# Optimization experiments

Measured on AMD Instinct MI355X. Metric: run time of the kernel, lower is better.

## Reference

```python
import jax, jax.numpy as jnp
import numpy as np

N_USERS = 200000
N_ITEMS = 100000
NNZ = 4000000
LATENT_DIM = 64
N_LAYERS = 3


def setup_inputs() -> dict:
    key = jax.random.key(0)
    k1, k2, k3, k4, k5 = jax.random.split(key, 5)
    N = N_USERS + N_ITEMS
    # nn.init.normal_(std=0.1) for both embedding tables
    user_emb = 0.1 * jax.random.normal(k1, (N_USERS, LATENT_DIM), dtype=jnp.float32)
    item_emb = 0.1 * jax.random.normal(k2, (N_ITEMS, LATENT_DIM), dtype=jnp.float32)
    # COO representation of the normalized sparse adjacency graph (getSparseGraph())
    vals = jax.random.uniform(k3, (NNZ,), dtype=jnp.float32)
    rows = jax.random.randint(k4, (NNZ,), 0, N, dtype=jnp.int32)
    cols = jax.random.randint(k5, (NNZ,), 0, N, dtype=jnp.int32)
    return {"user_emb": user_emb, "item_emb": item_emb, "vals": vals,
            "rows": rows, "cols": cols}


def reference(user_emb, item_emb, vals, rows, cols):
    """LightGCN.computer(): L rounds of SpMM propagation + mean over layers."""
    n_users = user_emb.shape[0]
    N = n_users + item_emb.shape[0]
    all_emb = jnp.concatenate([user_emb, item_emb], axis=0)  # [N, d]
    emb = all_emb
    acc = all_emb  # running sum of layer outputs (== mean of stacked embs * (L+1))
    for _ in range(N_LAYERS):
        # sparse.mm(G, emb): gather rows of emb at cols, scale by edge values,
        # scatter-add into destination rows.
        emb = jax.ops.segment_sum(vals[:, None] * emb[cols], rows, num_segments=N)
        acc = acc + emb
    light_out = acc / (N_LAYERS + 1)  # mean over (L+1) stacked layer embeddings
    users = light_out[:n_users]
    items = light_out[n_users:]
    return users, items
```

## Files before the change

kernel.cpp:

```cpp
#include <hip/hip_runtime.h>

#define N_USERS 200000
#define N_ITEMS 100000
#define NTOT    300000
#define NNZ     4000000
#define DIM     64
#define TOT_F   (NTOT * DIM)
#define TOT_F4  (TOT_F / 4)
#define USER_F4 ((N_USERS * DIM) / 4)

#define NCB     1172
#define CAP     3712
#define GPAD    16
#define NPB     250

typedef unsigned short ushort_t;
typedef unsigned long long u64_t;

__device__ __forceinline__ ushort_t f2bf(float f) {
    unsigned u = __float_as_uint(f);
    unsigned r = (u + 0x7FFFu + ((u >> 16) & 1u)) >> 16;
    return (ushort_t)r;
}

__global__ __launch_bounds__(256) void k_cvt(const float* __restrict__ ue,
                                             const float* __restrict__ ie,
                                             ushort_t* __restrict__ b0) {
    int i = blockIdx.x * blockDim.x + threadIdx.x;
    if (i >= TOT_F / 8) return;
    const float4* src = (i < USER_F4 / 2)
        ? reinterpret_cast<const float4*>(ue) + 2 * i
        : reinterpret_cast<const float4*>(ie) + 2 * i - USER_F4;
    float4 a = src[0], b = src[1];
    ushort_t o[8] = { f2bf(a.x), f2bf(a.y), f2bf(a.z), f2bf(a.w),
                      f2bf(b.x), f2bf(b.y), f2bf(b.z), f2bf(b.w) };
    reinterpret_cast<uint4*>(b0)[i] = *reinterpret_cast<uint4*>(o);
}


__global__ __launch_bounds__(256) void k_pb2(const int* __restrict__ rows,
                                             const int* __restrict__ cols,
                                             const float* __restrict__ vals,
                                             int* __restrict__ gcur,
                                             u64_t* __restrict__ bseg) {
    __shared__ int bh[NCB];
    int b = blockIdx.x, t = threadIdx.x;
    for (int i = t; i < NCB; i += 256) bh[i] = 0;
    __syncthreads();
    const int i0 = b * 4000, i1 = i0 + 4000;
    const int4* r4 = reinterpret_cast<const int4*>(rows);
    const int4* c4 = reinterpret_cast<const int4*>(cols);
    const float4* v4 = reinterpret_cast<const float4*>(vals);
    for (int i = i0 + t; i < i1; i += 256) {
        int4 r = r4[i];
        atomicAdd(&bh[r.x >> 8], 1);
        atomicAdd(&bh[r.y >> 8], 1);
        atomicAdd(&bh[r.z >> 8], 1);
        atomicAdd(&bh[r.w >> 8], 1);
    }
    __syncthreads();
    for (int k = t; k < NCB; k += 256) {
        int c = bh[k];
        bh[k] = c ? atomicAdd(&gcur[k * GPAD], c) : 0;
    }
    __syncthreads();
    for (int i = i0 + t; i < i1; i += 256) {
        int4   r = r4[i];
        int4   c = c4[i];
        float4 v = v4[i];
#define PUT(RR, CC, VV)                                                    \
        {                                                                  \
            int k = (RR) >> 8;                                             \
            int p = atomicAdd(&bh[k], 1);                                  \
            unsigned hi = (((unsigned)(RR) & 255u) << 24) | (unsigned)(CC);\
            bseg[(size_t)k * CAP + p] =                                    \
                ((u64_t)hi << 32) | (unsigned)__float_as_int(VV);          \
        }
        PUT(r.x, c.x, v.x)
        PUT(r.y, c.y, v.y)
        PUT(r.z, c.z, v.z)
        PUT(r.w, c.w, v.w)
#undef PUT
    }
}

__global__ __launch_bounds__(256) void k_rowsort(const int* __restrict__ gcur,
                                                 const u64_t* __restrict__ bseg,
                                                 long long* __restrict__ ecv,
                                                 int2* __restrict__ rstart2) {
    __shared__ int rh[256];
    __shared__ int rb[256];
    int b = blockIdx.x, t = threadIdx.x;
    int tot = gcur[b * GPAD];
    size_t segbase = (size_t)b * CAP;
    rh[t] = 0;
    __syncthreads();
    for (int e = t; e < tot; e += 256) {
        unsigned hi = (unsigned)(bseg[segbase + e] >> 32);
        atomicAdd(&rh[hi >> 24], 1);
    }
    __syncthreads();
    if (t == 0) {
        int run = 0;
        for (int i = 0; i < 256; ++i) { int c = rh[i]; rb[i] = run; run += c; }
    }
    __syncthreads();
    int row = b * 256 + t;
    if (row < NTOT)
        rstart2[row] = make_int2((int)segbase + rb[t],
                                 (int)segbase + rb[t] + rh[t]);
    rh[t] = rb[t];
    __syncthreads();
    for (int e = t; e < tot; e += 256) {
        u64_t q = bseg[segbase + e];
        unsigned hi = (unsigned)(q >> 32);
        int p = atomicAdd(&rh[hi >> 24], 1);
        ecv[segbase + p] = ((long long)((hi & 0x00FFFFFFu) << 7) << 32) |
                           (unsigned)q;
    }
    __syncthreads();
    if (t < 16 && tot + t < CAP) ecv[segbase + tot + t] = 0;
}


template<int LAYER>
__global__ __launch_bounds__(256) void k_spmm(const int2* __restrict__ rstart2,
                                              const long long* __restrict__ ecv,
                                              const ushort_t* __restrict__ src,
                                              const float* __restrict__ ue,
                                              const float* __restrict__ ie,
                                              ushort_t* __restrict__ dstb,
                                              float* __restrict__ out) {
    int wid  = blockIdx.x * 4 + (threadIdx.x >> 6);
    int lane = threadIdx.x & 63;
    if (wid >= NTOT) return;
    int2 se = rstart2[wid];
    int start = se.x, end = se.y;

    const int half = lane >> 5;
    const int d02  = (lane & 31) * 4;

    float acc0 = 0.f, acc1 = 0.f;
    long long q = ecv[start + (lane & 15)];
    for (int base = start; base < end; base += 16) {
        int rem = end - base;
        long long qn = q;
        if (rem > 16) qn = ecv[base + 16 + (lane & 15)];
        int qlo = (int)(unsigned)(q & 0xffffffffu);
        int qhi = (int)(unsigned)((unsigned long long)q >> 32);
        int remh = rem - half;
#pragma unroll
        for (int j = 0; j < 8; ++j) {
            int slot = 2 * j + half;
            float v  = __int_as_float(__shfl(qlo, slot));
            unsigned off = (unsigned)__shfl(qhi, slot);
            v = (2 * j < remh) ? v : 0.f;
            unsigned u = *reinterpret_cast<const unsigned*>(
                             reinterpret_cast<const char*>(src) + (off + d02));
            acc0 += v * __uint_as_float(u << 16);
            acc1 += v * __uint_as_float(u & 0xffff0000u);
        }
        q = qn;
    }

    acc0 += __shfl_xor(acc0, 32);
    acc1 += __shfl_xor(acc1, 32);

    if (lane < 32) {
        size_t o = (size_t)wid * DIM + (size_t)lane * 2;
        unsigned pk = ((unsigned)f2bf(acc1) << 16) | (unsigned)f2bf(acc0);
        if (LAYER == 1) {
            const float* bsrc = (wid < N_USERS)
                ? ue + o : ie + (o - (size_t)N_USERS * DIM);
            float2 b2 = *reinterpret_cast<const float2*>(bsrc);
            __builtin_nontemporal_store(b2.x + acc0, out + o);
            __builtin_nontemporal_store(b2.y + acc1, out + o + 1);
            *reinterpret_cast<unsigned*>(dstb + o) = pk;
        } else if (LAYER == 2) {
            float2 prev = *reinterpret_cast<const float2*>(out + o);
            __builtin_nontemporal_store(prev.x + acc0, out + o);
            __builtin_nontemporal_store(prev.y + acc1, out + o + 1);
            *reinterpret_cast<unsigned*>(dstb + o) = pk;
        } else {
            float2 prev = *reinterpret_cast<const float2*>(out + o);
            __builtin_nontemporal_store((prev.x + acc0) * 0.25f, out + o);
            __builtin_nontemporal_store((prev.y + acc1) * 0.25f, out + o + 1);
        }
    }
}


template<bool FROM_INPUTS>
__global__ __launch_bounds__(256) void scatter_kernel(
        const float* __restrict__ vals, const int* __restrict__ rows,
        const int* __restrict__ cols, const float* __restrict__ src,
        const float* __restrict__ ue, const float* __restrict__ ie,
        float* __restrict__ dst) {
    const int e = blockIdx.x * (blockDim.x >> 4) + (threadIdx.x >> 4);
    const int lane = threadIdx.x & 15;
    if (e >= NNZ) return;
    const float v = vals[e];
    const int c = cols[e];
    const int r = rows[e];
    const float* s = FROM_INPUTS
        ? ((c < N_USERS) ? (ue + (size_t)c * DIM) : (ie + (size_t)(c - N_USERS) * DIM))
        : (src + (size_t)c * DIM);
    const float4 x = reinterpret_cast<const float4*>(s)[lane];
    float* d = dst + (size_t)r * DIM + (size_t)lane * 4;
    atomicAdd(d + 0, v * x.x); atomicAdd(d + 1, v * x.y);
    atomicAdd(d + 2, v * x.z); atomicAdd(d + 3, v * x.w);
}

__global__ __launch_bounds__(256) void acc1_kernel(
        const float* __restrict__ ue, const float* __restrict__ ie,
        const float* __restrict__ a, float* __restrict__ out) {
    int i = blockIdx.x * blockDim.x + threadIdx.x;
    if (i >= TOT_F4) return;
    float4 base = (i < USER_F4)
        ? reinterpret_cast<const float4*>(ue)[i]
        : reinterpret_cast<const float4*>(ie)[i - USER_F4];
    float4 av = reinterpret_cast<const float4*>(a)[i];
    reinterpret_cast<float4*>(out)[i] =
        make_float4(base.x + av.x, base.y + av.y, base.z + av.z, base.w + av.w);
}

__global__ __launch_bounds__(256) void add_zero_kernel(
        const float* __restrict__ b, float* __restrict__ out,
        float* __restrict__ z) {
    int i = blockIdx.x * blockDim.x + threadIdx.x;
    if (i >= TOT_F4) return;
    float4 bv = reinterpret_cast<const float4*>(b)[i];
    float4 ov = reinterpret_cast<float4*>(out)[i];
    reinterpret_cast<float4*>(out)[i] =
        make_float4(ov.x + bv.x, ov.y + bv.y, ov.z + bv.z, ov.w + bv.w);
    reinterpret_cast<float4*>(z)[i] = make_float4(0.f, 0.f, 0.f, 0.f);
}

__global__ __launch_bounds__(256) void final_kernel(
        const float* __restrict__ b, float* __restrict__ out) {
    int i = blockIdx.x * blockDim.x + threadIdx.x;
    if (i >= TOT_F4) return;
    float4 bv = reinterpret_cast<const float4*>(b)[i];
    float4 ov = reinterpret_cast<float4*>(out)[i];
    reinterpret_cast<float4*>(out)[i] =
        make_float4((ov.x + bv.x) * 0.25f, (ov.y + bv.y) * 0.25f,
                    (ov.z + bv.z) * 0.25f, (ov.w + bv.w) * 0.25f);
}


extern "C" void kernel_launch(void* const* d_in, const int* in_sizes, int n_in,
                              void* d_out, int out_size, void* d_ws, size_t ws_size,
                              hipStream_t stream)
{
    const float* ue   = (const float*)d_in[0];
    const float* ie   = (const float*)d_in[1];
    const float* vals = (const float*)d_in[2];
    const int*   rows = (const int*)  d_in[3];
    const int*   cols = (const int*)  d_in[4];
    float* out = (float*)d_out;

    const size_t BBUF   = (size_t)TOT_F * 2;
    const size_t CAPTOT = (size_t)NCB * CAP;
    const size_t O_B1   = BBUF;
    const size_t O_B2   = 2 * BBUF;
    const size_t O_BSEG = O_B1;
    const size_t O_ECV  = 3 * BBUF;
    const size_t O_GC   = O_ECV + (CAPTOT + 32) * 8;
    const size_t O_RST  = O_GC + (size_t)NCB * GPAD * 4;
    const size_t NEED   = O_RST + (size_t)NTOT * 8 + 4096;

    if (ws_size >= NEED) {
        ushort_t*  b0     = (ushort_t*)d_ws;
        ushort_t*  b1     = (ushort_t*)((char*)d_ws + O_B1);
        ushort_t*  b2     = (ushort_t*)((char*)d_ws + O_B2);
        u64_t*     bseg   = (u64_t*)   ((char*)d_ws + O_BSEG);
        long long* ecv    = (long long*)((char*)d_ws + O_ECV);
        int*       gcur   = (int*)((char*)d_ws + O_GC);
        int2*      rstart2= (int2*)((char*)d_ws + O_RST);

        const int cg = (TOT_F / 8 + 255) / 256;
        const int sg = (NTOT + 3) / 4;

        hipMemsetAsync(gcur, 0, (size_t)NCB * GPAD * 4, stream);
        k_cvt<<<cg, 256, 0, stream>>>(ue, ie, b0);
        k_pb2<<<NPB, 256, 0, stream>>>(rows, cols, vals, gcur, bseg);
        k_rowsort<<<NCB, 256, 0, stream>>>(gcur, bseg, ecv, rstart2);

        k_spmm<1><<<sg, 256, 0, stream>>>(rstart2, ecv, b0, ue, ie, b1, out);
        k_spmm<2><<<sg, 256, 0, stream>>>(rstart2, ecv, b1, ue, ie, b2, out);
        k_spmm<3><<<sg, 256, 0, stream>>>(rstart2, ecv, b2, ue, ie, nullptr, out);
    } else {
        const size_t BUF = (size_t)TOT_F * sizeof(float);
        float* ws0 = (float*)d_ws;
        float* ws1 = (float*)((char*)d_ws + BUF);
        const int eb = 256;
        const int eg2 = (TOT_F4 + eb - 1) / eb;
        const int sg2 = (NNZ + 15) / 16;
        hipMemsetAsync(ws0, 0, BUF, stream);
        hipMemsetAsync(ws1, 0, BUF, stream);
        scatter_kernel<true><<<sg2, 256, 0, stream>>>(vals, rows, cols,
                                                      nullptr, ue, ie, ws0);
        acc1_kernel<<<eg2, eb, 0, stream>>>(ue, ie, ws0, out);
        scatter_kernel<false><<<sg2, 256, 0, stream>>>(vals, rows, cols,
                                                       ws0, nullptr, nullptr, ws1);
        add_zero_kernel<<<eg2, eb, 0, stream>>>(ws1, out, ws0);
        scatter_kernel<false><<<sg2, 256, 0, stream>>>(vals, rows, cols,
                                                       ws1, nullptr, nullptr, ws0);
        final_kernel<<<eg2, eb, 0, stream>>>(ws0, out);
    }
}
```

Baseline: 519.6 us.

## Quantize intermediate layer embeddings to int8 with per-row scales and fuse conversion

Layer 1 and 2 outputs are now stored as int8 with a per-row float scale instead of bf16, which halves the bytes each gathered neighbor row costs in layers 2 and 3. The bf16 conversion kernel is merged into the bucketing kernel as extra blocks, saving one launch. The SpMM inner loop now handles 32 edges per batch instead of 16, and the edge segments get extra padding so the wider reads stay in bounds. The cost is lower precision in the intermediate embeddings, plus one extra scale load per edge.

```diff
diff --git a/kernel.cpp b/kernel.cpp
--- a/kernel.cpp
+++ b/kernel.cpp
@@ -11,8 +11,10 @@
 
 #define NCB     1172
 #define CAP     3712
+#define CAP2    (CAP + 32)
 #define GPAD    16
 #define NPB     250
+#define CG      ((TOT_F / 8 + 255) / 256)
 
 typedef unsigned short ushort_t;
 typedef unsigned long long u64_t;
@@ -23,27 +25,28 @@
     return (ushort_t)r;
 }
 
-__global__ __launch_bounds__(256) void k_cvt(const float* __restrict__ ue,
-                                             const float* __restrict__ ie,
-                                             ushort_t* __restrict__ b0) {
-    int i = blockIdx.x * blockDim.x + threadIdx.x;
-    if (i >= TOT_F / 8) return;
-    const float4* src = (i < USER_F4 / 2)
-        ? reinterpret_cast<const float4*>(ue) + 2 * i
-        : reinterpret_cast<const float4*>(ie) + 2 * i - USER_F4;
-    float4 a = src[0], b = src[1];
-    ushort_t o[8] = { f2bf(a.x), f2bf(a.y), f2bf(a.z), f2bf(a.w),
-                      f2bf(b.x), f2bf(b.y), f2bf(b.z), f2bf(b.w) };
-    reinterpret_cast<uint4*>(b0)[i] = *reinterpret_cast<uint4*>(o);
-}
-
-
-__global__ __launch_bounds__(256) void k_pb2(const int* __restrict__ rows,
-                                             const int* __restrict__ cols,
-                                             const float* __restrict__ vals,
-                                             int* __restrict__ gcur,
-                                             u64_t* __restrict__ bseg) {
+
+__global__ __launch_bounds__(256) void k_build(const float* __restrict__ ue,
+                                               const float* __restrict__ ie,
+                                               const int* __restrict__ rows,
+                                               const int* __restrict__ cols,
+                                               const float* __restrict__ vals,
+                                               int* __restrict__ gcur,
+                                               u64_t* __restrict__ bseg,
+                                               ushort_t* __restrict__ b0) {
     __shared__ int bh[NCB];
+    if (blockIdx.x >= NPB) {
+        int i = (blockIdx.x - NPB) * 256 + threadIdx.x;
+        if (i >= TOT_F / 8) return;
+        const float4* src = (i < USER_F4 / 2)
+            ? reinterpret_cast<const float4*>(ue) + 2 * i
+            : reinterpret_cast<const float4*>(ie) + 2 * i - USER_F4;
+        float4 a = src[0], b = src[1];
+        ushort_t o[8] = { f2bf(a.x), f2bf(a.y), f2bf(a.z), f2bf(a.w),
+                          f2bf(b.x), f2bf(b.y), f2bf(b.z), f2bf(b.w) };
+        reinterpret_cast<uint4*>(b0)[i] = *reinterpret_cast<uint4*>(o);
+        return;
+    }
     int b = blockIdx.x, t = threadIdx.x;
     for (int i = t; i < NCB; i += 256) bh[i] = 0;
     __syncthreads();
@@ -92,7 +95,8 @@
     __shared__ int rb[256];
     int b = blockIdx.x, t = threadIdx.x;
     int tot = gcur[b * GPAD];
-    size_t segbase = (size_t)b * CAP;
+    size_t segbase  = (size_t)b * CAP;
+    size_t segbase2 = (size_t)b * CAP2;
     rh[t] = 0;
     __syncthreads();
     for (int e = t; e < tot; e += 256) {
@@ -107,30 +111,30 @@
     __syncthreads();
     int row = b * 256 + t;
     if (row < NTOT)
-        rstart2[row] = make_int2((int)segbase + rb[t],
-                                 (int)segbase + rb[t] + rh[t]);
+        rstart2[row] = make_int2((int)segbase2 + rb[t],
+                                 (int)segbase2 + rb[t] + rh[t]);
     rh[t] = rb[t];
     __syncthreads();
     for (int e = t; e < tot; e += 256) {
         u64_t q = bseg[segbase + e];
         unsigned hi = (unsigned)(q >> 32);
         int p = atomicAdd(&rh[hi >> 24], 1);
-        ecv[segbase + p] = ((long long)((hi & 0x00FFFFFFu) << 7) << 32) |
-                           (unsigned)q;
-    }
-    __syncthreads();
-    if (t < 16 && tot + t < CAP) ecv[segbase + tot + t] = 0;
-}
-
-
-template<int LAYER>
-__global__ __launch_bounds__(256) void k_spmm(const int2* __restrict__ rstart2,
-                                              const long long* __restrict__ ecv,
-                                              const ushort_t* __restrict__ src,
-                                              const float* __restrict__ ue,
-                                              const float* __restrict__ ie,
-                                              ushort_t* __restrict__ dstb,
-                                              float* __restrict__ out) {
+        ecv[segbase2 + p] = ((long long)((hi & 0x00FFFFFFu) << 7) << 32) |
+                            (unsigned)q;
+    }
+    __syncthreads();
+    if (t < 32) ecv[segbase2 + tot + t] = 0;
+}
+
+
+__global__ __launch_bounds__(256) void k_spmm1(const int2* __restrict__ rstart2,
+                                               const long long* __restrict__ ecv,
+                                               const ushort_t* __restrict__ src,
+                                               const float* __restrict__ ue,
+                                               const float* __restrict__ ie,
+                                               signed char* __restrict__ dstq,
+                                               float* __restrict__ dscale,
+                                               float* __restrict__ out) {
     int wid  = blockIdx.x * 4 + (threadIdx.x >> 6);
     int lane = threadIdx.x & 63;
     if (wid >= NTOT) return;
@@ -141,16 +145,16 @@
     const int d02  = (lane & 31) * 4;
 
     float acc0 = 0.f, acc1 = 0.f;
-    long long q = ecv[start + (lane & 15)];
-    for (int base = start; base < end; base += 16) {
+    long long q = ecv[start + (lane & 31)];
+    for (int base = start; base < end; base += 32) {
         int rem = end - base;
         long long qn = q;
-        if (rem > 16) qn = ecv[base + 16 + (lane & 15)];
+        if (rem > 32) qn = ecv[base + 32 + (lane & 31)];
         int qlo = (int)(unsigned)(q & 0xffffffffu);
         int qhi = (int)(unsigned)((unsigned long long)q >> 32);
         int remh = rem - half;
 #pragma unroll
-        for (int j = 0; j < 8; ++j) {
+        for (int j = 0; j < 16; ++j) {
             int slot = 2 * j + half;
             float v  = __int_as_float(__shfl(qlo, slot));
             unsigned off = (unsigned)__shfl(qhi, slot);
@@ -162,25 +166,92 @@
         }
         q = qn;
     }
-
     acc0 += __shfl_xor(acc0, 32);
     acc1 += __shfl_xor(acc1, 32);
 
+    float m = fmaxf(fabsf(acc0), fabsf(acc1));
+#pragma unroll
+    for (int d = 1; d < 32; d <<= 1) m = fmaxf(m, __shfl_xor(m, d));
+    float inv = (m > 1e-20f) ? 127.0f / m : 0.f;
+
     if (lane < 32) {
         size_t o = (size_t)wid * DIM + (size_t)lane * 2;
-        unsigned pk = ((unsigned)f2bf(acc1) << 16) | (unsigned)f2bf(acc0);
-        if (LAYER == 1) {
-            const float* bsrc = (wid < N_USERS)
-                ? ue + o : ie + (o - (size_t)N_USERS * DIM);
-            float2 b2 = *reinterpret_cast<const float2*>(bsrc);
-            __builtin_nontemporal_store(b2.x + acc0, out + o);
-            __builtin_nontemporal_store(b2.y + acc1, out + o + 1);
-            *reinterpret_cast<unsigned*>(dstb + o) = pk;
-        } else if (LAYER == 2) {
+        const float* bsrc = (wid < N_USERS)
+            ? ue + o : ie + (o - (size_t)N_USERS * DIM);
+        float2 b2 = *reinterpret_cast<const float2*>(bsrc);
+        __builtin_nontemporal_store(b2.x + acc0, out + o);
+        __builtin_nontemporal_store(b2.y + acc1, out + o + 1);
+        int q0 = (int)rintf(acc0 * inv);
+        int q1 = (int)rintf(acc1 * inv);
+        signed char pk[2] = { (signed char)q0, (signed char)q1 };
+        *reinterpret_cast<short*>(dstq + (size_t)wid * DIM + (lane & 31) * 2) =
+            *reinterpret_cast<const short*>(pk);
+        if (lane == 0) dscale[wid] = m * (1.0f / 127.0f);
+    }
+}
+
+
+template<int LAYER>
+__global__ __launch_bounds__(256) void k_spmm23(const int2* __restrict__ rstart2,
+                                                const long long* __restrict__ ecv,
+                                                const signed char* __restrict__ srcq,
+                                                const float* __restrict__ sscale,
+                                                signed char* __restrict__ dstq,
+                                                float* __restrict__ dscale,
+                                                float* __restrict__ out) {
+    int wid  = blockIdx.x * 4 + (threadIdx.x >> 6);
+    int lane = threadIdx.x & 63;
+    if (wid >= NTOT) return;
+    int2 se = rstart2[wid];
+    int start = se.x, end = se.y;
+
+    const int half = lane >> 5;
+    const int d01  = (lane & 31) * 2;
+
+    float acc0 = 0.f, acc1 = 0.f;
+    long long q = ecv[start + (lane & 31)];
+    for (int base = start; base < end; base += 32) {
+        int rem = end - base;
+        long long qn = q;
+        if (rem > 32) qn = ecv[base + 32 + (lane & 31)];
+        int qlo = (int)(unsigned)(q & 0xffffffffu);
+        int qhi = (int)(unsigned)((unsigned long long)q >> 32);
+        int remh = rem - half;
+#pragma unroll
+        for (int j = 0; j < 16; ++j) {
+            int slot = 2 * j + half;
+            float v  = __int_as_float(__shfl(qlo, slot));
+            unsigned off = (unsigned)__shfl(qhi, slot);
+            v = (2 * j < remh) ? v : 0.f;
+            float sc = sscale[off >> 7];
+            char2 c2 = *reinterpret_cast<const char2*>(
+                reinterpret_cast<const char*>(srcq) + ((off >> 1) + d01));
+            float mm = v * sc;
+            acc0 += mm * (float)c2.x;
+            acc1 += mm * (float)c2.y;
+        }
+        q = qn;
+    }
+    acc0 += __shfl_xor(acc0, 32);
+    acc1 += __shfl_xor(acc1, 32);
+
+    float m = fmaxf(fabsf(acc0), fabsf(acc1));
+#pragma unroll
+    for (int d = 1; d < 32; d <<= 1) m = fmaxf(m, __shfl_xor(m, d));
+    float inv = (m > 1e-20f) ? 127.0f / m : 0.f;
+
+    if (lane < 32) {
+        size_t o = (size_t)wid * DIM + (size_t)lane * 2;
+        if (LAYER == 2) {
             float2 prev = *reinterpret_cast<const float2*>(out + o);
             __builtin_nontemporal_store(prev.x + acc0, out + o);
             __builtin_nontemporal_store(prev.y + acc1, out + o + 1);
-            *reinterpret_cast<unsigned*>(dstb + o) = pk;
+            int q0 = (int)rintf(acc0 * inv);
+            int q1 = (int)rintf(acc1 * inv);
+            signed char pk[2] = { (signed char)q0, (signed char)q1 };
+            *reinterpret_cast<short*>(dstq + (size_t)wid * DIM + (lane & 31) * 2) =
+                *reinterpret_cast<const short*>(pk);
+            if (lane == 0) dscale[wid] = m * (1.0f / 127.0f);
         } else {
             float2 prev = *reinterpret_cast<const float2*>(out + o);
             __builtin_nontemporal_store((prev.x + acc0) * 0.25f, out + o);
@@ -259,36 +330,41 @@
     const int*   cols = (const int*)  d_in[4];
     float* out = (float*)d_out;
 
-    const size_t BBUF   = (size_t)TOT_F * 2;
-    const size_t CAPTOT = (size_t)NCB * CAP;
-    const size_t O_B1   = BBUF;
-    const size_t O_B2   = 2 * BBUF;
-    const size_t O_BSEG = O_B1;
-    const size_t O_ECV  = 3 * BBUF;
-    const size_t O_GC   = O_ECV + (CAPTOT + 32) * 8;
+    const size_t O_B0   = 0;
+    const size_t O_B1I  = 38400000;
+    const size_t O_B2I  = O_B1I + 19200000;
+    const size_t O_SC1  = O_B2I + 19200000;
+    const size_t O_SC2  = O_SC1 + 1200000;
+    const size_t O_BSEG = O_SC2 + 1200000;
+    const size_t O_ECV  = O_BSEG + (size_t)NCB * CAP * 8;
+    const size_t O_GC   = O_ECV + (size_t)NCB * CAP2 * 8;
     const size_t O_RST  = O_GC + (size_t)NCB * GPAD * 4;
     const size_t NEED   = O_RST + (size_t)NTOT * 8 + 4096;
 
     if (ws_size >= NEED) {
-        ushort_t*  b0     = (ushort_t*)d_ws;
-        ushort_t*  b1     = (ushort_t*)((char*)d_ws + O_B1);
-        ushort_t*  b2     = (ushort_t*)((char*)d_ws + O_B2);
-        u64_t*     bseg   = (u64_t*)   ((char*)d_ws + O_BSEG);
-        long long* ecv    = (long long*)((char*)d_ws + O_ECV);
-        int*       gcur   = (int*)((char*)d_ws + O_GC);
-        int2*      rstart2= (int2*)((char*)d_ws + O_RST);
-
-        const int cg = (TOT_F / 8 + 255) / 256;
+        ushort_t*    b0     = (ushort_t*)((char*)d_ws + O_B0);
+        signed char* b1i    = (signed char*)((char*)d_ws + O_B1I);
+        signed char* b2i    = (signed char*)((char*)d_ws + O_B2I);
+        float*       sc1    = (float*)((char*)d_ws + O_SC1);
+        float*       sc2    = (float*)((char*)d_ws + O_SC2);
+        u64_t*       bseg   = (u64_t*)((char*)d_ws + O_BSEG);
+        long long*   ecv    = (long long*)((char*)d_ws + O_ECV);
+        int*         gcur   = (int*)((char*)d_ws + O_GC);
+        int2*        rstart2= (int2*)((char*)d_ws + O_RST);
+
         const int sg = (NTOT + 3) / 4;
 
         hipMemsetAsync(gcur, 0, (size_t)NCB * GPAD * 4, stream);
-        k_cvt<<<cg, 256, 0, stream>>>(ue, ie, b0);
-        k_pb2<<<NPB, 256, 0, stream>>>(rows, cols, vals, gcur, bseg);
+        k_build<<<NPB + CG, 256, 0, stream>>>(ue, ie, rows, cols, vals,
+                                              gcur, bseg, b0);
         k_rowsort<<<NCB, 256, 0, stream>>>(gcur, bseg, ecv, rstart2);
 
-        k_spmm<1><<<sg, 256, 0, stream>>>(rstart2, ecv, b0, ue, ie, b1, out);
-        k_spmm<2><<<sg, 256, 0, stream>>>(rstart2, ecv, b1, ue, ie, b2, out);
-        k_spmm<3><<<sg, 256, 0, stream>>>(rstart2, ecv, b2, ue, ie, nullptr, out);
+        k_spmm1<<<sg, 256, 0, stream>>>(rstart2, ecv, b0, ue, ie,
+                                        b1i, sc1, out);
+        k_spmm23<2><<<sg, 256, 0, stream>>>(rstart2, ecv, b1i, sc1,
+                                            b2i, sc2, out);
+        k_spmm23<3><<<sg, 256, 0, stream>>>(rstart2, ecv, b2i, sc2,
+                                            nullptr, nullptr, out);
     } else {
         const size_t BUF = (size_t)TOT_F * sizeof(float);
         float* ws0 = (float*)d_ws;
```

New measurement: 597.9 us. 1.15x slower.
